# Performance work log

Hardware: AMD Instinct MI355X
Metric: run time of the kernel (lower is better)

Reference implementation:

```python
import jax, jax.numpy as jnp
import numpy as np

B, N = 4, 8192
D = 128
DEPTH = 4
LEAF = 32
HEADS = 4
HD = D // HEADS
SLOTS = 24
RANKS = [20, 32, 52, 82]                      # rank at encoder step j (fine -> coarse)
EXP = [RANKS[j] * (2 ** j) for j in range(DEPTH)]  # HODLR head output dims


def _rope_tables(seq_len, dim):
    inv_freq = 1.0 / (10000.0 ** (jnp.arange(0, dim, 2, dtype=jnp.float32) / dim))
    t = jnp.arange(seq_len, dtype=jnp.float32)
    freqs = t[:, None] * inv_freq[None, :]
    emb = jnp.concatenate([freqs, freqs], axis=-1)   # [S, dim]
    return jnp.cos(emb), jnp.sin(emb)


def _rotate_half(x):
    x1, x2 = jnp.split(x, 2, axis=-1)
    return jnp.concatenate([-x2, x1], axis=-1)


def _layernorm(x, g, b, eps=1e-5):
    mu = jnp.mean(x, -1, keepdims=True)
    var = jnp.mean((x - mu) ** 2, -1, keepdims=True)
    return (x - mu) * jax.lax.rsqrt(var + eps) * g + b


def _block_attn(h, qkv_w, qkv_b, pw, pb, cos, sin):
    Bc, Nc, C = h.shape
    nb = Nc // LEAF
    xb = h.reshape(Bc * nb, LEAF, C)
    qkv = (xb @ qkv_w + qkv_b).reshape(Bc * nb, LEAF, 3, HEADS, HD)
    qkv = qkv.transpose(2, 0, 3, 1, 4)               # [3, BN, H, L, hd]
    q, k, v = qkv[0], qkv[1], qkv[2]
    q = q * cos + _rotate_half(q) * sin              # full-dim RoPE (rope_dim == head_dim)
    k = k * cos + _rotate_half(k) * sin
    attn = jax.nn.softmax(jnp.einsum('bhqd,bhkd->bhqk', q, k) * (HD ** -0.5), axis=-1)
    o = jnp.einsum('bhqk,bhkd->bhqd', attn, v).transpose(0, 2, 1, 3).reshape(Bc * nb, LEAF, C)
    return (o @ pw + pb).reshape(Bc, Nc, C)


def _forward(x, cen_w, cen_b, nbr_w, nbr_b, inp_w, inp_b,
             leafp_w, leafp_b, leafh_w, leafh_b, log_scale_leaf,
             ln1_g, ln1_b, qkv_w, qkv_b, attnp_w, attnp_b,
             ln2_g, ln2_b, mlp1_w, mlp1_b, mlp2_w, mlp2_b, ds_w, ds_b,
             hu_w0, hu_b0, hv_w0, hv_b0, hu_w1, hu_b1, hv_w1, hv_b1,
             hu_w2, hu_b2, hv_w2, hv_b2, hu_w3, hu_b3, hv_w3, hv_b3):
    Bx, Nx, _ = x.shape
    # --- SymmetricNeighborEmbed (24 neighbor slots, vectorized) ---
    pos_i = x[..., 0:3]
    diag_i = x[..., 3:4]
    h_center = jnp.concatenate([pos_i, diag_i], -1) @ cen_w + cen_b          # [B,N,D]
    nb_feat = x[..., 4:4 + 5 * SLOTS].reshape(Bx, Nx, SLOTS, 5)
    rel = nb_feat[..., 0:1]
    pos_j = nb_feat[..., 1:4]
    w_ij = nb_feat[..., 4:5]
    active = (w_ij != 0.0).astype(x.dtype)
    feat = jnp.concatenate([rel * active, (pos_j - pos_i[:, :, None, :]) * active, w_ij], -1)
    e = (feat @ nbr_w + nbr_b) * active                                       # [B,N,24,D]
    h = h_center + jnp.sum(e, axis=2)
    h = h @ inp_w + inp_b
    # --- leaf dense diagonal blocks ---
    nl = Nx // LEAF
    hl = h.reshape(Bx, nl, LEAF, D) @ leafp_w + leafp_b                       # [B,nl,32,32]
    u_leaf = hl @ leafh_w + leafh_b
    dense = jnp.einsum('blik,bljk->blij', u_leaf, u_leaf) * jnp.exp(log_scale_leaf)
    diag_a = x[..., 3]                                                        # scale_A defaults to 1.0
    mask = jnp.abs(diag_a) > 1e-6
    new_diag = jnp.where(mask, 1.0 / jnp.where(mask, diag_a, 1.0), 1.0).reshape(Bx, nl, LEAF)
    dense = dense + new_diag[..., :, None] * jnp.eye(LEAF, dtype=x.dtype)
    # --- down-only encoder: transformer block -> HODLR head -> 2:1 downsample ---
    cos, sin = _rope_tables(LEAF, HD)
    hu = [(hu_w0, hu_b0), (hu_w1, hu_b1), (hu_w2, hu_b2), (hu_w3, hu_b3)]
    hv = [(hv_w0, hv_b0), (hv_w1, hv_b1), (hv_w2, hv_b2), (hv_w3, hv_b3)]
    us, vs = [], []
    for j in range(DEPTH):
        a = _block_attn(_layernorm(h, ln1_g[j], ln1_b[j]),
                        qkv_w[j], qkv_b[j], attnp_w[j], attnp_b[j], cos, sin)
        h = h + a
        m = _layernorm(h, ln2_g[j], ln2_b[j])
        m = jax.nn.gelu(m @ mlp1_w[j] + mlp1_b[j], approximate=False) @ mlp2_w[j] + mlp2_b[j]
        h = h + m
        us.append((h @ hu[j][0] + hu[j][1]).reshape(Bx, Nx, RANKS[j]))
        vs.append((h @ hv[j][0] + hv[j][1]).reshape(Bx, Nx, RANKS[j]))
        Bh, n, c = h.shape
        h = h.reshape(Bh, n // 2, 2 * c) @ ds_w[j] + ds_b[j]
    # single flat output: dense leaf blocks + all U/V HODLR factors
    return jnp.concatenate([dense.reshape(Bx, -1),
                            jnp.concatenate(us, -1).reshape(Bx, -1),
                            jnp.concatenate(vs, -1).reshape(Bx, -1)], -1)


def setup_inputs():
    key = jax.random.key(0)
    ks = iter(jax.random.split(key, 64))
    def rn(shape, s=0.05):
        return jax.random.normal(next(ks), shape, jnp.float32) * s
    z = lambda *s: jnp.zeros(s, jnp.float32)
    o = lambda *s: jnp.ones(s, jnp.float32)
    inp = {
        'x': jax.random.normal(next(ks), (B, N, 4 + 5 * SLOTS), jnp.float32),
        'cen_w': rn((4, D)), 'cen_b': z(D),
        'nbr_w': rn((5, D)), 'nbr_b': z(D),
        'inp_w': rn((D, D)), 'inp_b': z(D),
        'leafp_w': rn((D, LEAF)), 'leafp_b': z(LEAF),
        'leafh_w': rn((LEAF, LEAF), 0.01), 'leafh_b': z(LEAF),
        'log_scale_leaf': jnp.full((1,), np.log(0.01), jnp.float32),
        'ln1_g': o(DEPTH, D), 'ln1_b': z(DEPTH, D),
        'qkv_w': rn((DEPTH, D, 3 * D)), 'qkv_b': z(DEPTH, 3 * D),
        'attnp_w': rn((DEPTH, D, D)), 'attnp_b': z(DEPTH, D),
        'ln2_g': o(DEPTH, D), 'ln2_b': z(DEPTH, D),
        'mlp1_w': rn((DEPTH, D, 4 * D)), 'mlp1_b': z(DEPTH, 4 * D),
        'mlp2_w': rn((DEPTH, 4 * D, D)), 'mlp2_b': z(DEPTH, D),
        'ds_w': rn((DEPTH, 2 * D, D)), 'ds_b': z(DEPTH, D),
    }
    for j in range(DEPTH):
        inp['hu_w%d' % j] = rn((D, EXP[j]), 0.01)
        inp['hu_b%d' % j] = z(EXP[j])
        inp['hv_w%d' % j] = rn((D, EXP[j]), 0.01)
        inp['hv_b%d' % j] = z(EXP[j])
    return inp


def reference(x, cen_w, cen_b, nbr_w, nbr_b, inp_w, inp_b,
              leafp_w, leafp_b, leafh_w, leafh_b, log_scale_leaf,
              ln1_g, ln1_b, qkv_w, qkv_b, attnp_w, attnp_b,
              ln2_g, ln2_b, mlp1_w, mlp1_b, mlp2_w, mlp2_b, ds_w, ds_b,
              hu_w0, hu_b0, hv_w0, hv_b0, hu_w1, hu_b1, hv_w1, hv_b1,
              hu_w2, hu_b2, hv_w2, hv_b2, hu_w3, hu_b3, hv_w3, hv_b3):
    return _forward(x, cen_w, cen_b, nbr_w, nbr_b, inp_w, inp_b,
                    leafp_w, leafp_b, leafh_w, leafh_b, log_scale_leaf,
                    ln1_g, ln1_b, qkv_w, qkv_b, attnp_w, attnp_b,
                    ln2_g, ln2_b, mlp1_w, mlp1_b, mlp2_w, mlp2_b, ds_w, ds_b,
                    hu_w0, hu_b0, hv_w0, hv_b0, hu_w1, hu_b1, hv_w1, hv_b1,
                    hu_w2, hu_b2, hv_w2, hv_b2, hu_w3, hu_b3, hv_w3, hv_b3)
```

## Files before the change

kernel.cpp:

```cpp
#include <hip/hip_runtime.h>
#include <math.h>

#define DEV __device__ __forceinline__

constexpr int XFv = 124;
constexpr size_t OPB   = 3309568;
constexpr size_t UBASE = 262144;
constexpr size_t VBASE = 1785856;
constexpr int UVWID = 186;

using bfrag  = __attribute__((ext_vector_type(8))) short;
using f32x4v = __attribute__((ext_vector_type(4))) float;

DEV float* at4p(float* base, int t, int c0, int W) {
  return base + t * W + ((c0 + 4 * t) & (W - 1));
}
DEV float& at1r(float* base, int t, int c, int W) {
  return base[t * W + (((c & ~3) + 4 * t) & (W - 1)) + (c & 3)];
}
DEV float4 ld4g(const float* p) { return *(const float4*)p; }
DEV void fma4(float4& a, float s, const float4& w) {
  a.x += s * w.x; a.y += s * w.y; a.z += s * w.z; a.w += s * w.w;
}
DEV float gelu_fast(float x) {
// ... 66 lines not shown
  S[1280 + tid] = cb[tid];
  __syncthreads();
  float acc[11];
#pragma unroll
  for (int r = 0; r < 10; r++) acc[r] = 0.f;
  acc[10] = ib[tid];
  for (int k = 0; k < 128; k++) {
    float w = iw[k * 128 + tid];
#pragma unroll
    for (int r = 0; r < 11; r++) acc[r] += S[r * 128 + k] * w;
  }
#pragma unroll
  for (int r = 0; r < 11; r++) weff[r * 128 + tid] = acc[r];
  for (int idx = tid; idx < 512; idx += 128) {
    int pos = idx >> 4, d = idx & 15;
    float ang = (float)pos * expf(-0.57564627324851148f * (float)d);
    ropetab[idx] = cosf(ang);
    ropetab[512 + idx] = sinf(ang);
  }
}

__global__ __launch_bounds__(256) void node_embed2_kernel(
    const float* __restrict__ x, const float* __restrict__ weff,
    float* __restrict__ h) {
  __shared__ float XR[64 * XFv];
  __shared__ float RF[64][11];
  __shared__ __align__(16) float WE[11 * 128];
  int tid = threadIdx.x;
  int node0 = blockIdx.x * 64;
  for (int i = tid; i < 64 * XFv; i += 256)
    XR[i] = x[(size_t)node0 * XFv + i];
  for (int i = tid; i < 11 * 128; i += 256) WE[i] = weff[i];
  __syncthreads();
  {
    int nn = tid >> 2, sl = tid & 3;
    const float* xr = XR + nn * XFv;
    float p0 = xr[0], p1 = xr[1], p2 = xr[2];
    float g[6] = {0.f, 0.f, 0.f, 0.f, 0.f, 0.f};
#pragma unroll
    for (int s = 0; s < 6; s++) {
      const float* f = xr + 4 + 5 * (sl * 6 + s);
      float w = f[4];
      if (w != 0.0f) {
        g[0] += f[0]; g[1] += f[1] - p0; g[2] += f[2] - p1;
        g[3] += f[3] - p2; g[4] += w; g[5] += 1.0f;
      }
    }
#pragma unroll
    for (int i = 0; i < 6; i++) {
      g[i] += __shfl_xor(g[i], 1);
      g[i] += __shfl_xor(g[i], 2);
    }
    if (sl == 0) {
      RF[nn][0] = p0; RF[nn][1] = p1; RF[nn][2] = p2; RF[nn][3] = xr[3];
#pragma unroll
      for (int i = 0; i < 6; i++) RF[nn][4 + i] = g[i];
    }
  }
  __syncthreads();
  {
    int w = tid >> 6, lane = tid & 63;
    int c4 = lane & 31, hi = lane >> 5;
    const float4* WE4 = (const float4*)WE;
#pragma unroll
    for (int rr = 0; rr < 8; rr++) {
      int node = w * 16 + rr * 2 + hi;
      float4 acc = WE4[10 * 32 + c4];
#pragma unroll
      for (int f = 0; f < 10; f++)
        fma4(acc, RF[node][f], WE4[f * 32 + c4]);
      *(float4*)&h[(size_t)(node0 + node) * 128 + c4 * 4] = acc;
    }
  }
}

__global__ __launch_bounds__(256) void leaf_dense_kernel(
    const float* __restrict__ h, const float* __restrict__ x,
    const float* __restrict__ lpw, const float* __restrict__ lpb,
    const float* __restrict__ lhw, const float* __restrict__ lhb,
    const float* __restrict__ lsc, float* __restrict__ out) {
  __shared__ __align__(16) float HS[32 * 128];
  __shared__ __align__(16) float HL[32 * 32];
  __shared__ __align__(16) float UL[32 * 32];
  int tid = threadIdx.x;
  int leaf = blockIdx.x;
  size_t base = (size_t)leaf * (32 * 128);
  for (int i = tid; i < 32 * 128; i += 256) {
    int t = i >> 7, c = i & 127;
    at1r(HS, t, c, 128) = h[base + i];
  }
  __syncthreads();
  int t = tid & 31, cg = tid >> 5;
  {
    float4 acc = ld4g(&lpb[4 * cg]);
    for (int k4 = 0; k4 < 128; k4 += 4) {
      float4 xv = *(const float4*)at4p(HS, t, k4, 128);
      float xa[4] = {xv.x, xv.y, xv.z, xv.w};
#pragma unroll
      for (int kk = 0; kk < 4; kk++)
        fma4(acc, xa[kk], ld4g(&lpw[(k4 + kk) * 32 + 4 * cg]));
    }
    *(float4*)at4p(HL, t, 4 * cg, 32) = acc;
  }
  __syncthreads();
  {
    float4 acc = ld4g(&lhb[4 * cg]);
    for (int k4 = 0; k4 < 32; k4 += 4) {
      float4 xv = *(const float4*)at4p(HL, t, k4, 32);
      float xa[4] = {xv.x, xv.y, xv.z, xv.w};
#pragma unroll
      for (int kk = 0; kk < 4; kk++)
        fma4(acc, xa[kk], ld4g(&lhw[(k4 + kk) * 32 + 4 * cg]));
    }
    *(float4*)at4p(UL, t, 4 * cg, 32) = acc;
  }
  __syncthreads();
  {
    float scale = expf(lsc[0]);
    float acc[4] = {0.f, 0.f, 0.f, 0.f};
    for (int k4 = 0; k4 < 32; k4 += 4) {
      float4 xv = *(const float4*)at4p(UL, t, k4, 32);
      float xa[4] = {xv.x, xv.y, xv.z, xv.w};
#pragma unroll
      for (int kk = 0; kk < 4; kk++) {
        int k = k4 + kk;
#pragma unroll
        for (int i2 = 0; i2 < 4; i2++)
          acc[i2] += xa[kk] * at1r(UL, 4 * cg + i2, k, 32);
      }
    }
    int b = leaf >> 8, l = leaf & 255;
#pragma unroll
    for (int i2 = 0; i2 < 4; i2++) {
      int c = 4 * cg + i2;
      float v = acc[i2] * scale;
      if (c == t) {
        float dg = x[(size_t)(leaf * 32 + t) * XFv + 3];
        v += (fabsf(dg) > 1e-6f) ? (1.0f / dg) : 1.0f;
      }
      out[(size_t)b * OPB + (size_t)l * 1024 + t * 32 + c] = v;
    }
  }
}

__global__ __launch_bounds__(256, 4) void layer_mfma_kernel(
    float* __restrict__ h,
    const float* __restrict__ lng, const float* __restrict__ lnb,
    const ushort* __restrict__ wqkvt, const float* __restrict__ bqkv,
    const ushort* __restrict__ wpt, const float* __restrict__ pb,
    const float* __restrict__ rt,
    const float* __restrict__ ln2g, const float* __restrict__ ln2b,
    const ushort* __restrict__ w1t, const float* __restrict__ b1,
    const ushort* __restrict__ w2t, const float* __restrict__ b2) {
  __shared__ __align__(16) ushort SM[16384];
  ushort* XN = SM;
  ushort* QB = SM + 4096;
  ushort* KB = SM + 8192;
  ushort* VT = SM + 12288;
  float*  HS = (float*)(SM + 8192);
  int tid = threadIdx.x;
  size_t base = (size_t)blockIdx.x * (32 * 128);

  {
    int m = tid >> 3, p = tid & 7;
    const float* row = h + base + m * 128 + p * 16;
    float v[16];
    float s = 0.f;
#pragma unroll
    for (int i = 0; i < 16; i += 4) {
      float4 t4 = ld4g(row + i);
      v[i] = t4.x; v[i + 1] = t4.y; v[i + 2] = t4.z; v[i + 3] = t4.w;
      s += t4.x + t4.y + t4.z + t4.w;
    }
    s += __shfl_xor(s, 1); s += __shfl_xor(s, 2); s += __shfl_xor(s, 4);
    float mu = s * (1.0f / 128.0f);
    float s2 = 0.f;
#pragma unroll
    for (int i = 0; i < 16; i++) { float d = v[i] - mu; s2 += d * d; }
    s2 += __shfl_xor(s2, 1); s2 += __shfl_xor(s2, 2); s2 += __shfl_xor(s2, 4);
    float rs = rsqrtf(s2 * (1.0f / 128.0f) + 1e-5f);
    unsigned* XW = (unsigned*)XN;
#pragma unroll
    for (int i = 0; i < 16; i += 2) {
      int c = p * 16 + i;
      float x0 = (v[i] - mu) * rs * lng[c] + lnb[c];
      float x1 = (v[i + 1] - mu) * rs * lng[c + 1] + lnb[c + 1];
      int kp = c >> 1;
      XW[m * 64 + ((kp + 4 * m) & 63)] =
          (unsigned)f2bf(x0) | ((unsigned)f2bf(x1) << 16);
    }
  }
  __syncthreads();

  int w = tid >> 6, l = tid & 63, lm = l & 15, q = l >> 4;

  {
    f32x4v acc[2][6];
#pragma unroll
    for (int mt = 0; mt < 2; mt++)
#pragma unroll
      for (int nt = 0; nt < 6; nt++) acc[mt][nt] = (f32x4v){0.f, 0.f, 0.f, 0.f};
    for (int ks = 0; ks < 4; ks++) {
      bfrag a[2];
#pragma unroll
      for (int mt = 0; mt < 2; mt++) {
        int mm = mt * 16 + lm;
        a[mt] = *(const bfrag*)&XN[mm * 128 + ((ks * 32 + q * 8 + 8 * mm) & 127)];
      }
#pragma unroll
      for (int nt = 0; nt < 6; nt++) {
        int n = w * 96 + nt * 16 + lm;
        bfrag b = *(const bfrag*)&wqkvt[(size_t)n * 128 + ks * 32 + q * 8];
#pragma unroll
        for (int mt = 0; mt < 2; mt++)
          acc[mt][nt] = __builtin_amdgcn_mfma_f32_16x16x32_bf16(
              a[mt], b, acc[mt][nt], 0, 0, 0);
      }
    }
    float csA[4] = {}, snA[4] = {}, csB[4] = {}, snB[4] = {};
    if (w < 3) {
#pragma unroll
      for (int r = 0; r < 4; r++) {
        int pa = q * 4 + r;
        csA[r] = rt[pa * 16 + lm];        snA[r] = rt[512 + pa * 16 + lm];
        csB[r] = rt[(pa + 16) * 16 + lm]; snB[r] = rt[512 + (pa + 16) * 16 + lm];
      }
    }
#pragma unroll
    for (int p2 = 0; p2 < 3; p2++) {
      int g = w * 6 + 2 * p2;
      int ne = g * 16 + lm;
      if (g < 16) {
        float be = bqkv[ne], bo = bqkv[ne + 16];
        ushort* dst = (g < 8) ? QB : KB;
        int de = (g < 8) ? ne : ne - 128;
#pragma unroll
        for (int mt = 0; mt < 2; mt++)
#pragma unroll
          for (int r = 0; r < 4; r++) {
            int mm = mt * 16 + q * 4 + r;
            float cs = (mt & 1) ? csB[r] : csA[r];
            float sn = (mt & 1) ? snB[r] : snA[r];
            float e = acc[mt][2 * p2][r] + be;
            float o = acc[mt][2 * p2 + 1][r] + bo;
            stb128(dst, mm, de, e * cs - o * sn);
            stb128(dst, mm, de + 16, o * cs + e * sn);
          }
      } else {
#pragma unroll
        for (int h2 = 0; h2 < 2; h2++) {
          int nt = 2 * p2 + h2;
          int nv = (g + h2) * 16 + lm;
          int dv = nv - 256;
          float bv = bqkv[nv];
#pragma unroll
          for (int mt = 0; mt < 2; mt++) {
            int t0 = mt * 16 + q * 4;
            short4 pk;
            pk.x = (short)f2bf(acc[mt][nt][0] + bv);
            pk.y = (short)f2bf(acc[mt][nt][1] + bv);
            pk.z = (short)f2bf(acc[mt][nt][2] + bv);
            pk.w = (short)f2bf(acc[mt][nt][3] + bv);
            *(short4*)&VT[dv * 32 + (((t0 & ~7) + 8 * dv) & 31) + (t0 & 7)] = pk;
          }
        }
      }
    }
  }
  __syncthreads();

  ushort* SP = XN;
  {
    int head = w;
    f32x4v sc[2][2];
#pragma unroll
    for (int a2 = 0; a2 < 2; a2++)
#pragma unroll
      for (int b2 = 0; b2 < 2; b2++) sc[a2][b2] = (f32x4v){0.f, 0.f, 0.f, 0.f};
    bfrag qa[2], kb[2];
#pragma unroll
    for (int mt2 = 0; mt2 < 2; mt2++) {
      int row = mt2 * 16 + lm;
      qa[mt2] = *(const bfrag*)&QB[row * 128 + ((head * 32 + q * 8 + 8 * row) & 127)];
    }
#pragma unroll
    for (int nt2 = 0; nt2 < 2; nt2++) {
      int kt = nt2 * 16 + lm;
      kb[nt2] = *(const bfrag*)&KB[kt * 128 + ((head * 32 + q * 8 + 8 * kt) & 127)];
    }
#pragma unroll
    for (int mt2 = 0; mt2 < 2; mt2++)
#pragma unroll
      for (int nt2 = 0; nt2 < 2; nt2++)
        sc[mt2][nt2] = __builtin_amdgcn_mfma_f32_16x16x32_bf16(
            qa[mt2], kb[nt2], sc[mt2][nt2], 0, 0, 0);
    const float scl = 0.17677669529663688f;
#pragma unroll
    for (int mt2 = 0; mt2 < 2; mt2++)
#pragma unroll
      for (int nt2 = 0; nt2 < 2; nt2++)
#pragma unroll
        for (int r = 0; r < 4; r++) {
          int qt = mt2 * 16 + q * 4 + r;
          int kc = nt2 * 16 + lm;
          SP[head * 1024 + qt * 32 + (((kc & ~7) + 8 * qt) & 31) + (kc & 7)] =
              f2bf(sc[mt2][nt2][r] * scl);
        }
  }
  __syncthreads();

  {
    if (tid < 128) {
      int head = tid >> 5, qt = tid & 31;
      ushort* rowp = SP + head * 1024 + qt * 32;
      float v[32];
#pragma unroll
      for (int pc = 0; pc < 4; pc++) {
        uint4 ch = *(const uint4*)&rowp[pc * 8];
        unsigned uu[4] = {ch.x, ch.y, ch.z, ch.w};
#pragma unroll
        for (int i2 = 0; i2 < 4; i2++) {
          v[pc * 8 + 2 * i2]     = __uint_as_float(uu[i2] << 16);
          v[pc * 8 + 2 * i2 + 1] = __uint_as_float(uu[i2] & 0xffff0000u);
        }
      }
      float mx = -1e30f;
#pragma unroll
      for (int i = 0; i < 32; i++) mx = fmaxf(mx, v[i]);
      float s = 0.f;
#pragma unroll
      for (int i = 0; i < 32; i++) { v[i] = __expf(v[i] - mx); s += v[i]; }
      float inv = 1.0f / s;
#pragma unroll
      for (int pc = 0; pc < 4; pc++) {
        uint4 ch;
        unsigned uu[4];
#pragma unroll
        for (int i2 = 0; i2 < 4; i2++)
          uu[i2] = (unsigned)f2bf(v[pc * 8 + 2 * i2] * inv) |
                   ((unsigned)f2bf(v[pc * 8 + 2 * i2 + 1] * inv) << 16);
        ch.x = uu[0]; ch.y = uu[1]; ch.z = uu[2]; ch.w = uu[3];
        *(uint4*)&rowp[pc * 8] = ch;
      }
    }
  }
  __syncthreads();

  ushort* OB = QB;
  {
    int head = w;
    f32x4v ov[2][2];
#pragma unroll
    for (int a2 = 0; a2 < 2; a2++)
#pragma unroll
      for (int b2 = 0; b2 < 2; b2++) ov[a2][b2] = (f32x4v){0.f, 0.f, 0.f, 0.f};
    bfrag pa[2], vb2[2];
#pragma unroll
    for (int mt2 = 0; mt2 < 2; mt2++) {
      int qt = mt2 * 16 + lm;
      pa[mt2] = *(const bfrag*)&SP[head * 1024 + qt * 32 + ((q * 8 + 8 * qt) & 31)];
    }
#pragma unroll
    for (int nt2 = 0; nt2 < 2; nt2++) {
      int gdim = head * 32 + nt2 * 16 + lm;
      vb2[nt2] = *(const bfrag*)&VT[gdim * 32 + ((q * 8 + 8 * gdim) & 31)];
    }
#pragma unroll
    for (int mt2 = 0; mt2 < 2; mt2++)
#pragma unroll
      for (int nt2 = 0; nt2 < 2; nt2++)
        ov[mt2][nt2] = __builtin_amdgcn_mfma_f32_16x16x32_bf16(
            pa[mt2], vb2[nt2], ov[mt2][nt2], 0, 0, 0);
#pragma unroll
    for (int mt2 = 0; mt2 < 2; mt2++)
#pragma unroll
      for (int nt2 = 0; nt2 < 2; nt2++)
#pragma unroll
        for (int r = 0; r < 4; r++) {
          int qt = mt2 * 16 + q * 4 + r;
          int gdim = head * 32 + nt2 * 16 + lm;
          stb128(OB, qt, gdim, ov[mt2][nt2][r]);
        }
  }
  __syncthreads();

  {
    f32x4v po[2][2];
#pragma unroll
    for (int mt = 0; mt < 2; mt++)
#pragma unroll
      for (int nt = 0; nt < 2; nt++) po[mt][nt] = (f32x4v){0.f, 0.f, 0.f, 0.f};
    for (int ks = 0; ks < 4; ks++) {
      bfrag a[2];
#pragma unroll
      for (int mt = 0; mt < 2; mt++) {
        int mm = mt * 16 + lm;
        a[mt] = *(const bfrag*)&OB[mm * 128 + ((ks * 32 + q * 8 + 8 * mm) & 127)];
      }
#pragma unroll
      for (int nt = 0; nt < 2; nt++) {
        int n = w * 32 + nt * 16 + lm;
        bfrag b = *(const bfrag*)&wpt[(size_t)n * 128 + ks * 32 + q * 8];
#pragma unroll
        for (int mt = 0; mt < 2; mt++)
          po[mt][nt] = __builtin_amdgcn_mfma_f32_16x16x32_bf16(
              a[mt], b, po[mt][nt], 0, 0, 0);
      }
    }
#pragma unroll
    for (int nt = 0; nt < 2; nt++) {
      int n = w * 32 + nt * 16 + lm;
      float bv = pb[n];
#pragma unroll
      for (int mt = 0; mt < 2; mt++)
#pragma unroll
        for (int r = 0; r < 4; r++) {
          int mm = mt * 16 + q * 4 + r;
          at1r(HS, mm, n, 128) = po[mt][nt][r] + bv;
        }
    }
  }
  __syncthreads();

  {
    int j = tid & 31;
    int c0 = j * 4;
    float g0 = ln2g[c0], g1 = ln2g[c0 + 1], g2 = ln2g[c0 + 2], g3 = ln2g[c0 + 3];
    float e0 = ln2b[c0], e1 = ln2b[c0 + 1], e2 = ln2b[c0 + 2], e3 = ln2b[c0 + 3];
    unsigned* XW = (unsigned*)XN;
#pragma unroll
    for (int k2 = 0; k2 < 4; k2++) {
      int idx = tid + 256 * k2;
      int tok = idx >> 5;
      float4 hg = ld4g(&h[base + (size_t)idx * 4]);
      float4 ao = *(const float4*)at4p(HS, tok, 4 * j, 128);
      float4 hn;
      hn.x = hg.x + ao.x; hn.y = hg.y + ao.y;
      hn.z = hg.z + ao.z; hn.w = hg.w + ao.w;
      *(float4*)at4p(HS, tok, 4 * j, 128) = hn;
      float s = hn.x + hn.y + hn.z + hn.w;
      s += __shfl_xor(s, 1); s += __shfl_xor(s, 2); s += __shfl_xor(s, 4);
      s += __shfl_xor(s, 8); s += __shfl_xor(s, 16);
      float mu = s * (1.0f / 128.0f);
      float d0 = hn.x - mu, d1 = hn.y - mu, d2 = hn.z - mu, d3 = hn.w - mu;
      float s2 = d0 * d0 + d1 * d1 + d2 * d2 + d3 * d3;
      s2 += __shfl_xor(s2, 1); s2 += __shfl_xor(s2, 2); s2 += __shfl_xor(s2, 4);
      s2 += __shfl_xor(s2, 8); s2 += __shfl_xor(s2, 16);
      float rs = rsqrtf(s2 * (1.0f / 128.0f) + 1e-5f);
      float x0 = d0 * rs * g0 + e0;
      float x1 = d1 * rs * g1 + e1;
      float x2 = d2 * rs * g2 + e2;
      float x3 = d3 * rs * g3 + e3;
      int kp = 2 * j;
      XW[tok * 64 + ((kp + 4 * tok) & 63)] =
          (unsigned)f2bf(x0) | ((unsigned)f2bf(x1) << 16);
      XW[tok * 64 + ((kp + 1 + 4 * tok) & 63)] =
          (unsigned)f2bf(x2) | ((unsigned)f2bf(x3) << 16);
    }
  }
  __syncthreads();

  ushort* HC = QB;
  f32x4v acc2[2][2];
#pragma unroll
  for (int mt = 0; mt < 2; mt++)
#pragma unroll
    for (int nt = 0; nt < 2; nt++) acc2[mt][nt] = (f32x4v){0.f, 0.f, 0.f, 0.f};

  for (int hc = 0; hc < 4; hc++) {
    f32x4v acc1[2][2];
#pragma unroll
    for (int mt = 0; mt < 2; mt++)
#pragma unroll
      for (int nt = 0; nt < 2; nt++) acc1[mt][nt] = (f32x4v){0.f, 0.f, 0.f, 0.f};
#pragma unroll
    for (int ks = 0; ks < 4; ks++) {
      bfrag a[2];
#pragma unroll
      for (int mt = 0; mt < 2; mt++) {
        int mm = mt * 16 + lm;
        a[mt] = *(const bfrag*)&XN[mm * 128 + ((ks * 32 + q * 8 + 8 * mm) & 127)];
      }
#pragma unroll
      for (int nt = 0; nt < 2; nt++) {
        int n = hc * 128 + w * 32 + nt * 16 + lm;
        bfrag b = *(const bfrag*)&w1t[(size_t)n * 128 + ks * 32 + q * 8];
#pragma unroll
        for (int mt = 0; mt < 2; mt++)
          acc1[mt][nt] = __builtin_amdgcn_mfma_f32_16x16x32_bf16(
              a[mt], b, acc1[mt][nt], 0, 0, 0);
      }
    }
    if (hc) __syncthreads();
#pragma unroll
    for (int nt = 0; nt < 2; nt++) {
      int nl = w * 32 + nt * 16 + lm;
      float b1v = b1[hc * 128 + nl];
#pragma unroll
      for (int mt = 0; mt < 2; mt++)
#pragma unroll
        for (int r = 0; r < 4; r++) {
          int mm = mt * 16 + q * 4 + r;
          float val = gelu_fast(acc1[mt][nt][r] + b1v);
          HC[mm * 128 + (((nl & ~7) + 8 * mm) & 127) + (nl & 7)] = f2bf(val);
        }
    }
    __syncthreads();
#pragma unroll
    for (int ks = 0; ks < 4; ks++) {
      bfrag a[2];
#pragma unroll
      for (int mt = 0; mt < 2; mt++) {
        int mm = mt * 16 + lm;
        a[mt] = *(const bfrag*)&HC[mm * 128 + ((ks * 32 + q * 8 + 8 * mm) & 127)];
      }
#pragma unroll
      for (int nt = 0; nt < 2; nt++) {
        int n = w * 32 + nt * 16 + lm;
        bfrag b = *(const bfrag*)&w2t[(size_t)n * 512 + hc * 128 + ks * 32 + q * 8];
#pragma unroll
        for (int mt = 0; mt < 2; mt++)
          acc2[mt][nt] = __builtin_amdgcn_mfma_f32_16x16x32_bf16(
              a[mt], b, acc2[mt][nt], 0, 0, 0);
      }
    }
  }

#pragma unroll
  for (int nt = 0; nt < 2; nt++) {
    int n = w * 32 + nt * 16 + lm;
    float b2v = b2[n];
#pragma unroll
    for (int mt = 0; mt < 2; mt++)
#pragma unroll
      for (int r = 0; r < 4; r++) {
        int mm = mt * 16 + q * 4 + r;
        h[base + (size_t)mm * 128 + n] = at1r(HS, mm, n, 128) + acc2[mt][nt][r] + b2v;
      }
  }
}

template <int EXPJ, int RANK, int LVL, int NSPLIT>
__global__ __launch_bounds__(256) void uvds_kernel(
    const float* __restrict__ h,
    const ushort* __restrict__ uwt, const float* __restrict__ ub,
    const ushort* __restrict__ vwt, const float* __restrict__ vb,
    float* __restrict__ ustg, float* __restrict__ vstg,
    float* __restrict__ hout,
    const ushort* __restrict__ dwt, const float* __restrict__ dsb) {
  constexpr int NT16 = (EXPJ + 15) / 16;
  constexpr int NJOBS = 2 * NT16;
  __shared__ __align__(16) ushort XN[64 * 128];
  int tid = threadIdx.x;
  int t0 = blockIdx.x * 64;
  size_t base = (size_t)t0 * 128;
  {
    int m = tid >> 2, p = tid & 3;
    const float* row = h + base + m * 128 + p * 32;
    unsigned* XW = (unsigned*)XN;
#pragma unroll
    for (int i = 0; i < 32; i += 4) {
      float4 t4 = ld4g(row + i);
      int kp = (p * 32 + i) >> 1;
      XW[m * 64 + ((kp + 4 * m) & 63)] =
          (unsigned)f2bf(t4.x) | ((unsigned)f2bf(t4.y) << 16);
      XW[m * 64 + ((kp + 1 + 4 * m) & 63)] =
          (unsigned)f2bf(t4.z) | ((unsigned)f2bf(t4.w) << 16);
    }
  }
  __syncthreads();
  int w = tid >> 6, l = tid & 63, lm = l & 15, q = l >> 4;
  int gw = w + 4 * blockIdx.y;
  for (int jj = gw; jj < NJOBS; jj += 4 * NSPLIT) {
    int uvsel = jj & 1, nt = jj >> 1;
    const ushort* wt = uvsel ? vwt : uwt;
    const float* bias = uvsel ? vb : ub;
    float* stg = uvsel ? vstg : ustg;
    f32x4v acc[4];
#pragma unroll
    for (int mt = 0; mt < 4; mt++) acc[mt] = (f32x4v){0.f, 0.f, 0.f, 0.f};
    for (int ks = 0; ks < 4; ks++) {
      bfrag b = *(const bfrag*)&wt[(size_t)(nt * 16 + lm) * 128 + ks * 32 + q * 8];
#pragma unroll
      for (int mt = 0; mt < 4; mt++) {
        int mm = mt * 16 + lm;
        int ke = ks * 32 + q * 8;
        bfrag a = *(const bfrag*)&XN[mm * 128 + ((ke + 8 * mm) & 127)];
        acc[mt] = __builtin_amdgcn_mfma_f32_16x16x32_bf16(a, b, acc[mt], 0, 0, 0);
      }
    }
    int c = nt * 16 + lm;
    if (c < EXPJ) {
      float bv = bias[c];
#pragma unroll
      for (int mt = 0; mt < 4; mt++)
#pragma unroll
        for (int r = 0; r < 4; r++) {
          int mm = mt * 16 + q * 4 + r;
          stg[(size_t)(t0 + mm) * EXPJ + c] = acc[mt][r] + bv;
        }
    }
  }
  if constexpr (LVL < 3) {
    if (blockIdx.y == 0) {
      f32x4v dacc[2][2];
#pragma unroll
      for (int mt = 0; mt < 2; mt++)
#pragma unroll
        for (int nt = 0; nt < 2; nt++) dacc[mt][nt] = (f32x4v){0.f, 0.f, 0.f, 0.f};
      for (int ks = 0; ks < 8; ks++) {
        bfrag a[2];
#pragma unroll
        for (int mt = 0; mt < 2; mt++) {
          int rr = mt * 16 + lm;
          int tok = 2 * rr + (ks >> 2);
          int c2 = (ks & 3) * 32 + q * 8;
          a[mt] = *(const bfrag*)&XN[tok * 128 + ((c2 + 8 * tok) & 127)];
        }
#pragma unroll
        for (int nt = 0; nt < 2; nt++) {
          int n = w * 32 + nt * 16 + lm;
          bfrag b = *(const bfrag*)&dwt[(size_t)n * 256 + ks * 32 + q * 8];
#pragma unroll
          for (int mt = 0; mt < 2; mt++)
            dacc[mt][nt] = __builtin_amdgcn_mfma_f32_16x16x32_bf16(
                a[mt], b, dacc[mt][nt], 0, 0, 0);
        }
      }
      size_t ob2 = (size_t)blockIdx.x * (32 * 128);
#pragma unroll
      for (int nt = 0; nt < 2; nt++) {
        int n = w * 32 + nt * 16 + lm;
        float bv = dsb[n];
#pragma unroll
        for (int mt = 0; mt < 2; mt++)
#pragma unroll
          for (int r = 0; r < 4; r++) {
            int mm = mt * 16 + q * 4 + r;
            hout[ob2 + (size_t)mm * 128 + n] = dacc[mt][nt][r] + bv;
          }
      }
    }
  }
}

struct StgPtrs { const float* u[4]; const float* v[4]; };
__global__ __launch_bounds__(256) void uv_assemble_kernel(
    StgPtrs sp, float* __restrict__ out) {
  __shared__ unsigned char JL[93];
  __shared__ unsigned char CM[93];
  int tid = threadIdx.x;
  if (tid < 93) {
    int c = 2 * tid;
    int j = (c < 20) ? 0 : (c < 52) ? 1 : (c < 104) ? 2 : 3;
    int coff = (j == 0) ? 0 : (j == 1) ? 20 : (j == 2) ? 52 : 104;
    JL[tid] = (unsigned char)j;
    CM[tid] = (unsigned char)(c - coff);
  }
  __syncthreads();
  int g0 = blockIdx.x * 32;
  for (int i = tid; i < 32 * 93; i += 256) {
    int rr = i / 93, cp = i - rr * 93;
    int g = g0 + rr;
    int b = g >> 13, n = g & 8191;
    int j = JL[cp], cm = CM[cp];
    int expj, rank;
    if (j == 0)      { expj = 20;  rank = 20; }
    else if (j == 1) { expj = 64;  rank = 32; }
    else if (j == 2) { expj = 208; rank = 52; }
    else             { expj = 656; rank = 82; }
    int tok = (b << (13 - j)) + (n >> j);
    int cdiv = n & ((1 << j) - 1);
    size_t si = (size_t)tok * expj + cdiv * rank + cm;
    size_t ob = (size_t)b * OPB + (size_t)n * UVWID + 2 * cp;
    *(float2*)&out[ob + UBASE] = *(const float2*)&sp.u[j][si];
    *(float2*)&out[ob + VBASE] = *(const float2*)&sp.v[j][si];
  }
}

// ... 127 lines not shown
```

Baseline: 441.0 us.

## Double-buffer MLP hidden chunks and prefetch weight fragments in fused layer kernel

Restructures the transformer layer kernel's MLP into a software pipeline. A second LDS buffer holds GELU chunks, so the next chunk's first matmul overlaps the previous chunk's second matmul and the loop needs one fewer barrier per chunk. It also prefetches proj and first MLP1 weight fragments into registers before the attention stages, keeps the input residual in registers instead of reloading it from global for LN2, and splits softmax rows across two threads so all 256 threads work. LDS rises from 32KB to 40KB and register pressure grows, which may reduce occupancy under launch_bounds(256,4).

```diff
diff --git a/kernel.cpp b/kernel.cpp
--- a/kernel.cpp
+++ b/kernel.cpp
@@ -242,47 +242,47 @@
     const float* __restrict__ ln2g, const float* __restrict__ ln2b,
     const ushort* __restrict__ w1t, const float* __restrict__ b1,
     const ushort* __restrict__ w2t, const float* __restrict__ b2) {
-  __shared__ __align__(16) ushort SM[16384];
+  __shared__ __align__(16) ushort SM[20480];
   ushort* XN = SM;
   ushort* QB = SM + 4096;
   ushort* KB = SM + 8192;
   ushort* VT = SM + 12288;
+  ushort* HC1 = SM + 16384;
   float*  HS = (float*)(SM + 8192);
   int tid = threadIdx.x;
   size_t base = (size_t)blockIdx.x * (32 * 128);
-
-  {
-    int m = tid >> 3, p = tid & 7;
-    const float* row = h + base + m * 128 + p * 16;
-    float v[16];
+  int m8 = tid >> 3, p8 = tid & 7;
+  int w = tid >> 6, l = tid & 63, lm = l & 15, q = l >> 4;
+  float hreg[16];
+
+  {
+    const float* row = h + base + m8 * 128 + p8 * 16;
     float s = 0.f;
 #pragma unroll
     for (int i = 0; i < 16; i += 4) {
       float4 t4 = ld4g(row + i);
-      v[i] = t4.x; v[i + 1] = t4.y; v[i + 2] = t4.z; v[i + 3] = t4.w;
+      hreg[i] = t4.x; hreg[i + 1] = t4.y; hreg[i + 2] = t4.z; hreg[i + 3] = t4.w;
       s += t4.x + t4.y + t4.z + t4.w;
     }
     s += __shfl_xor(s, 1); s += __shfl_xor(s, 2); s += __shfl_xor(s, 4);
     float mu = s * (1.0f / 128.0f);
     float s2 = 0.f;
 #pragma unroll
-    for (int i = 0; i < 16; i++) { float d = v[i] - mu; s2 += d * d; }
+    for (int i = 0; i < 16; i++) { float d = hreg[i] - mu; s2 += d * d; }
     s2 += __shfl_xor(s2, 1); s2 += __shfl_xor(s2, 2); s2 += __shfl_xor(s2, 4);
     float rs = rsqrtf(s2 * (1.0f / 128.0f) + 1e-5f);
     unsigned* XW = (unsigned*)XN;
 #pragma unroll
     for (int i = 0; i < 16; i += 2) {
-      int c = p * 16 + i;
-      float x0 = (v[i] - mu) * rs * lng[c] + lnb[c];
-      float x1 = (v[i + 1] - mu) * rs * lng[c + 1] + lnb[c + 1];
+      int c = p8 * 16 + i;
+      float x0 = (hreg[i] - mu) * rs * lng[c] + lnb[c];
+      float x1 = (hreg[i + 1] - mu) * rs * lng[c + 1] + lnb[c + 1];
       int kp = c >> 1;
-      XW[m * 64 + ((kp + 4 * m) & 63)] =
+      XW[m8 * 64 + ((kp + 4 * m8) & 63)] =
           (unsigned)f2bf(x0) | ((unsigned)f2bf(x1) << 16);
     }
   }
   __syncthreads();
-
-  int w = tid >> 6, l = tid & 63, lm = l & 15, q = l >> 4;
 
   {
     f32x4v acc[2][6];
@@ -359,6 +359,15 @@
   }
   __syncthreads();
 
+  bfrag pfF[4][2];
+#pragma unroll
+  for (int ks = 0; ks < 4; ks++)
+#pragma unroll
+    for (int nt = 0; nt < 2; nt++) {
+      int n = w * 32 + nt * 16 + lm;
+      pfF[ks][nt] = *(const bfrag*)&wpt[(size_t)n * 128 + ks * 32 + q * 8];
+    }
+
   ushort* SP = XN;
   {
     int head = w;
@@ -400,38 +409,39 @@
   __syncthreads();
 
   {
-    if (tid < 128) {
-      int head = tid >> 5, qt = tid & 31;
-      ushort* rowp = SP + head * 1024 + qt * 32;
-      float v[32];
-#pragma unroll
-      for (int pc = 0; pc < 4; pc++) {
-        uint4 ch = *(const uint4*)&rowp[pc * 8];
-        unsigned uu[4] = {ch.x, ch.y, ch.z, ch.w};
-#pragma unroll
-        for (int i2 = 0; i2 < 4; i2++) {
-          v[pc * 8 + 2 * i2]     = __uint_as_float(uu[i2] << 16);
-          v[pc * 8 + 2 * i2 + 1] = __uint_as_float(uu[i2] & 0xffff0000u);
-        }
-      }
-      float mx = -1e30f;
-#pragma unroll
-      for (int i = 0; i < 32; i++) mx = fmaxf(mx, v[i]);
-      float s = 0.f;
-#pragma unroll
-      for (int i = 0; i < 32; i++) { v[i] = __expf(v[i] - mx); s += v[i]; }
-      float inv = 1.0f / s;
-#pragma unroll
-      for (int pc = 0; pc < 4; pc++) {
-        uint4 ch;
-        unsigned uu[4];
-#pragma unroll
-        for (int i2 = 0; i2 < 4; i2++)
-          uu[i2] = (unsigned)f2bf(v[pc * 8 + 2 * i2] * inv) |
-                   ((unsigned)f2bf(v[pc * 8 + 2 * i2 + 1] * inv) << 16);
-        ch.x = uu[0]; ch.y = uu[1]; ch.z = uu[2]; ch.w = uu[3];
-        *(uint4*)&rowp[pc * 8] = ch;
-      }
+    int rowid = tid >> 1, half = tid & 1;
+    int head = rowid >> 5, qt = rowid & 31;
+    ushort* rowp = SP + head * 1024 + qt * 32 + half * 16;
+    float v[16];
+#pragma unroll
+    for (int pc = 0; pc < 2; pc++) {
+      uint4 ch = *(const uint4*)&rowp[pc * 8];
+      unsigned uu[4] = {ch.x, ch.y, ch.z, ch.w};
+#pragma unroll
+      for (int i2 = 0; i2 < 4; i2++) {
+        v[pc * 8 + 2 * i2]     = __uint_as_float(uu[i2] << 16);
+        v[pc * 8 + 2 * i2 + 1] = __uint_as_float(uu[i2] & 0xffff0000u);
+      }
+    }
+    float mx = -1e30f;
+#pragma unroll
+    for (int i = 0; i < 16; i++) mx = fmaxf(mx, v[i]);
+    mx = fmaxf(mx, __shfl_xor(mx, 1));
+    float s = 0.f;
+#pragma unroll
+    for (int i = 0; i < 16; i++) { v[i] = __expf(v[i] - mx); s += v[i]; }
+    s += __shfl_xor(s, 1);
+    float inv = 1.0f / s;
+#pragma unroll
+    for (int pc = 0; pc < 2; pc++) {
+      uint4 ch;
+      unsigned uu[4];
+#pragma unroll
+      for (int i2 = 0; i2 < 4; i2++)
+        uu[i2] = (unsigned)f2bf(v[pc * 8 + 2 * i2] * inv) |
+                 ((unsigned)f2bf(v[pc * 8 + 2 * i2 + 1] * inv) << 16);
+      ch.x = uu[0]; ch.y = uu[1]; ch.z = uu[2]; ch.w = uu[3];
+      *(uint4*)&rowp[pc * 8] = ch;
     }
   }
   __syncthreads();
@@ -480,6 +490,7 @@
     for (int mt = 0; mt < 2; mt++)
 #pragma unroll
       for (int nt = 0; nt < 2; nt++) po[mt][nt] = (f32x4v){0.f, 0.f, 0.f, 0.f};
+#pragma unroll
     for (int ks = 0; ks < 4; ks++) {
       bfrag a[2];
 #pragma unroll
@@ -488,14 +499,11 @@
         a[mt] = *(const bfrag*)&OB[mm * 128 + ((ks * 32 + q * 8 + 8 * mm) & 127)];
       }
 #pragma unroll
-      for (int nt = 0; nt < 2; nt++) {
-        int n = w * 32 + nt * 16 + lm;
-        bfrag b = *(const bfrag*)&wpt[(size_t)n * 128 + ks * 32 + q * 8];
+      for (int nt = 0; nt < 2; nt++)
 #pragma unroll
         for (int mt = 0; mt < 2; mt++)
           po[mt][nt] = __builtin_amdgcn_mfma_f32_16x16x32_bf16(
-              a[mt], b, po[mt][nt], 0, 0, 0);
-      }
+              a[mt], pfF[ks][nt], po[mt][nt], 0, 0, 0);
     }
 #pragma unroll
     for (int nt = 0; nt < 2; nt++) {
@@ -512,57 +520,63 @@
   }
   __syncthreads();
 
-  {
-    int j = tid & 31;
-    int c0 = j * 4;
-    float g0 = ln2g[c0], g1 = ln2g[c0 + 1], g2 = ln2g[c0 + 2], g3 = ln2g[c0 + 3];
-    float e0 = ln2b[c0], e1 = ln2b[c0 + 1], e2 = ln2b[c0 + 2], e3 = ln2b[c0 + 3];
+  bfrag pfW1[4][2];
+#pragma unroll
+  for (int ks = 0; ks < 4; ks++)
+#pragma unroll
+    for (int nt = 0; nt < 2; nt++) {
+      int n = w * 32 + nt * 16 + lm;
+      pfW1[ks][nt] = *(const bfrag*)&w1t[(size_t)n * 128 + ks * 32 + q * 8];
+    }
+
+  {
+    float s = 0.f;
+    float hn[16];
+#pragma unroll
+    for (int i = 0; i < 16; i += 4) {
+      float4 ao = *(const float4*)at4p(HS, m8, p8 * 16 + i, 128);
+      hn[i] = hreg[i] + ao.x;     hn[i + 1] = hreg[i + 1] + ao.y;
+      hn[i + 2] = hreg[i + 2] + ao.z; hn[i + 3] = hreg[i + 3] + ao.w;
+      s += hn[i] + hn[i + 1] + hn[i + 2] + hn[i + 3];
+    }
+    s += __shfl_xor(s, 1); s += __shfl_xor(s, 2); s += __shfl_xor(s, 4);
+    float mu = s * (1.0f / 128.0f);
+    float s2 = 0.f;
+#pragma unroll
+    for (int i = 0; i < 16; i++) { float d = hn[i] - mu; s2 += d * d; }
+    s2 += __shfl_xor(s2, 1); s2 += __shfl_xor(s2, 2); s2 += __shfl_xor(s2, 4);
+    float rs = rsqrtf(s2 * (1.0f / 128.0f) + 1e-5f);
+#pragma unroll
+    for (int i = 0; i < 16; i += 4) {
+      float4 w4;
+      w4.x = hn[i]; w4.y = hn[i + 1]; w4.z = hn[i + 2]; w4.w = hn[i + 3];
+      *(float4*)at4p(HS, m8, p8 * 16 + i, 128) = w4;
+    }
     unsigned* XW = (unsigned*)XN;
 #pragma unroll
-    for (int k2 = 0; k2 < 4; k2++) {
-      int idx = tid + 256 * k2;
-      int tok = idx >> 5;
-      float4 hg = ld4g(&h[base + (size_t)idx * 4]);
-      float4 ao = *(const float4*)at4p(HS, tok, 4 * j, 128);
-      float4 hn;
-      hn.x = hg.x + ao.x; hn.y = hg.y + ao.y;
-      hn.z = hg.z + ao.z; hn.w = hg.w + ao.w;
-      *(float4*)at4p(HS, tok, 4 * j, 128) = hn;
-      float s = hn.x + hn.y + hn.z + hn.w;
-      s += __shfl_xor(s, 1); s += __shfl_xor(s, 2); s += __shfl_xor(s, 4);
-      s += __shfl_xor(s, 8); s += __shfl_xor(s, 16);
-      float mu = s * (1.0f / 128.0f);
-      float d0 = hn.x - mu, d1 = hn.y - mu, d2 = hn.z - mu, d3 = hn.w - mu;
-      float s2 = d0 * d0 + d1 * d1 + d2 * d2 + d3 * d3;
-      s2 += __shfl_xor(s2, 1); s2 += __shfl_xor(s2, 2); s2 += __shfl_xor(s2, 4);
-      s2 += __shfl_xor(s2, 8); s2 += __shfl_xor(s2, 16);
-      float rs = rsqrtf(s2 * (1.0f / 128.0f) + 1e-5f);
-      float x0 = d0 * rs * g0 + e0;
-      float x1 = d1 * rs * g1 + e1;
-      float x2 = d2 * rs * g2 + e2;
-      float x3 = d3 * rs * g3 + e3;
-      int kp = 2 * j;
-      XW[tok * 64 + ((kp + 4 * tok) & 63)] =
+    for (int i = 0; i < 16; i += 2) {
+      int c = p8 * 16 + i;
+      float x0 = (hn[i] - mu) * rs * ln2g[c] + ln2b[c];
+      float x1 = (hn[i + 1] - mu) * rs * ln2g[c + 1] + ln2b[c + 1];
+      int kp = c >> 1;
+      XW[m8 * 64 + ((kp + 4 * m8) & 63)] =
           (unsigned)f2bf(x0) | ((unsigned)f2bf(x1) << 16);
-      XW[tok * 64 + ((kp + 1 + 4 * tok) & 63)] =
-          (unsigned)f2bf(x2) | ((unsigned)f2bf(x3) << 16);
-    }
-  }
-  __syncthreads();
-
-  ushort* HC = QB;
+    }
+  }
+  __syncthreads();
+
+  ushort* HC0 = QB;
   f32x4v acc2[2][2];
 #pragma unroll
   for (int mt = 0; mt < 2; mt++)
 #pragma unroll
     for (int nt = 0; nt < 2; nt++) acc2[mt][nt] = (f32x4v){0.f, 0.f, 0.f, 0.f};
 
-  for (int hc = 0; hc < 4; hc++) {
-    f32x4v acc1[2][2];
+  auto mlp1_calc = [&](int hc, f32x4v A1[2][2]) {
 #pragma unroll
     for (int mt = 0; mt < 2; mt++)
 #pragma unroll
-      for (int nt = 0; nt < 2; nt++) acc1[mt][nt] = (f32x4v){0.f, 0.f, 0.f, 0.f};
+      for (int nt = 0; nt < 2; nt++) A1[mt][nt] = (f32x4v){0.f, 0.f, 0.f, 0.f};
 #pragma unroll
     for (int ks = 0; ks < 4; ks++) {
       bfrag a[2];
@@ -577,11 +591,12 @@
         bfrag b = *(const bfrag*)&w1t[(size_t)n * 128 + ks * 32 + q * 8];
 #pragma unroll
         for (int mt = 0; mt < 2; mt++)
-          acc1[mt][nt] = __builtin_amdgcn_mfma_f32_16x16x32_bf16(
-              a[mt], b, acc1[mt][nt], 0, 0, 0);
-      }
-    }
-    if (hc) __syncthreads();
+          A1[mt][nt] = __builtin_amdgcn_mfma_f32_16x16x32_bf16(
+              a[mt], b, A1[mt][nt], 0, 0, 0);
+      }
+    }
+  };
+  auto gelu_store = [&](int hc, f32x4v A1[2][2], ushort* HCd) {
 #pragma unroll
     for (int nt = 0; nt < 2; nt++) {
       int nl = w * 32 + nt * 16 + lm;
@@ -591,18 +606,19 @@
 #pragma unroll
         for (int r = 0; r < 4; r++) {
           int mm = mt * 16 + q * 4 + r;
-          float val = gelu_fast(acc1[mt][nt][r] + b1v);
-          HC[mm * 128 + (((nl & ~7) + 8 * mm) & 127) + (nl & 7)] = f2bf(val);
+          float val = gelu_fast(A1[mt][nt][r] + b1v);
+          HCd[mm * 128 + (((nl & ~7) + 8 * mm) & 127) + (nl & 7)] = f2bf(val);
         }
     }
-    __syncthreads();
+  };
+  auto mlp2_calc = [&](int hc, ushort* HCr) {
 #pragma unroll
     for (int ks = 0; ks < 4; ks++) {
       bfrag a[2];
 #pragma unroll
       for (int mt = 0; mt < 2; mt++) {
         int mm = mt * 16 + lm;
-        a[mt] = *(const bfrag*)&HC[mm * 128 + ((ks * 32 + q * 8 + 8 * mm) & 127)];
+        a[mt] = *(const bfrag*)&HCr[mm * 128 + ((ks * 32 + q * 8 + 8 * mm) & 127)];
       }
 #pragma unroll
       for (int nt = 0; nt < 2; nt++) {
@@ -614,7 +630,45 @@
               a[mt], b, acc2[mt][nt], 0, 0, 0);
       }
     }
-  }
+  };
+
+  f32x4v a1A[2][2], a1B[2][2];
+  {
+#pragma unroll
+    for (int mt = 0; mt < 2; mt++)
+#pragma unroll
+      for (int nt = 0; nt < 2; nt++) a1A[mt][nt] = (f32x4v){0.f, 0.f, 0.f, 0.f};
+#pragma unroll
+    for (int ks = 0; ks < 4; ks++) {
+      bfrag a[2];
+#pragma unroll
+      for (int mt = 0; mt < 2; mt++) {
+        int mm = mt * 16 + lm;
+        a[mt] = *(const bfrag*)&XN[mm * 128 + ((ks * 32 + q * 8 + 8 * mm) & 127)];
+      }
+#pragma unroll
+      for (int nt = 0; nt < 2; nt++)
+#pragma unroll
+        for (int mt = 0; mt < 2; mt++)
+          a1A[mt][nt] = __builtin_amdgcn_mfma_f32_16x16x32_bf16(
+              a[mt], pfW1[ks][nt], a1A[mt][nt], 0, 0, 0);
+    }
+  }
+  gelu_store(0, a1A, HC0);
+  __syncthreads();
+  mlp1_calc(1, a1B);
+  mlp2_calc(0, HC0);
+  gelu_store(1, a1B, HC1);
+  __syncthreads();
+  mlp1_calc(2, a1A);
+  mlp2_calc(1, HC1);
+  gelu_store(2, a1A, HC0);
+  __syncthreads();
+  mlp1_calc(3, a1B);
+  mlp2_calc(2, HC0);
+  gelu_store(3, a1B, HC1);
+  __syncthreads();
+  mlp2_calc(3, HC1);
 
 #pragma unroll
   for (int nt = 0; nt < 2; nt++) {
```

After: 434.9 us. No clear change (-1.4%).

## Double-buffer MLP hidden chunks and split softmax rows across thread pairs

Applied to the files above, without the earlier changes.

The MLP loop now ping-pongs between two LDS buffers for the GELU hidden chunk. This lets the next chunk's first GEMM be issued alongside the current chunk's second GEMM, and drops from two barriers per chunk to one. Softmax now uses all 256 threads, with two threads per row combining max and sum through shuffles, instead of 128 idle-half threads. LDS per block grows from 32 KB to 40 KB, which may reduce occupancy under the 4-blocks launch bound.

```diff
diff --git a/kernel.cpp b/kernel.cpp
--- a/kernel.cpp
+++ b/kernel.cpp
@@ -242,18 +242,20 @@
     const float* __restrict__ ln2g, const float* __restrict__ ln2b,
     const ushort* __restrict__ w1t, const float* __restrict__ b1,
     const ushort* __restrict__ w2t, const float* __restrict__ b2) {
-  __shared__ __align__(16) ushort SM[16384];
+  __shared__ __align__(16) ushort SM[20480];
   ushort* XN = SM;
   ushort* QB = SM + 4096;
   ushort* KB = SM + 8192;
   ushort* VT = SM + 12288;
+  ushort* HC1 = SM + 16384;
   float*  HS = (float*)(SM + 8192);
   int tid = threadIdx.x;
   size_t base = (size_t)blockIdx.x * (32 * 128);
-
-  {
-    int m = tid >> 3, p = tid & 7;
-    const float* row = h + base + m * 128 + p * 16;
+  int w = tid >> 6, l = tid & 63, lm = l & 15, q = l >> 4;
+
+  {
+    int m8 = tid >> 3, p8 = tid & 7;
+    const float* row = h + base + m8 * 128 + p8 * 16;
     float v[16];
     float s = 0.f;
 #pragma unroll
@@ -272,17 +274,15 @@
     unsigned* XW = (unsigned*)XN;
 #pragma unroll
     for (int i = 0; i < 16; i += 2) {
-      int c = p * 16 + i;
+      int c = p8 * 16 + i;
       float x0 = (v[i] - mu) * rs * lng[c] + lnb[c];
       float x1 = (v[i + 1] - mu) * rs * lng[c + 1] + lnb[c + 1];
       int kp = c >> 1;
-      XW[m * 64 + ((kp + 4 * m) & 63)] =
+      XW[m8 * 64 + ((kp + 4 * m8) & 63)] =
           (unsigned)f2bf(x0) | ((unsigned)f2bf(x1) << 16);
     }
   }
   __syncthreads();
-
-  int w = tid >> 6, l = tid & 63, lm = l & 15, q = l >> 4;
 
   {
     f32x4v acc[2][6];
@@ -400,38 +400,39 @@
   __syncthreads();
 
   {
-    if (tid < 128) {
-      int head = tid >> 5, qt = tid & 31;
-      ushort* rowp = SP + head * 1024 + qt * 32;
-      float v[32];
-#pragma unroll
-      for (int pc = 0; pc < 4; pc++) {
-        uint4 ch = *(const uint4*)&rowp[pc * 8];
-        unsigned uu[4] = {ch.x, ch.y, ch.z, ch.w};
-#pragma unroll
-        for (int i2 = 0; i2 < 4; i2++) {
-          v[pc * 8 + 2 * i2]     = __uint_as_float(uu[i2] << 16);
-          v[pc * 8 + 2 * i2 + 1] = __uint_as_float(uu[i2] & 0xffff0000u);
-        }
-      }
-      float mx = -1e30f;
-#pragma unroll
-      for (int i = 0; i < 32; i++) mx = fmaxf(mx, v[i]);
-      float s = 0.f;
-#pragma unroll
-      for (int i = 0; i < 32; i++) { v[i] = __expf(v[i] - mx); s += v[i]; }
-      float inv = 1.0f / s;
-#pragma unroll
-      for (int pc = 0; pc < 4; pc++) {
-        uint4 ch;
-        unsigned uu[4];
-#pragma unroll
-        for (int i2 = 0; i2 < 4; i2++)
-          uu[i2] = (unsigned)f2bf(v[pc * 8 + 2 * i2] * inv) |
-                   ((unsigned)f2bf(v[pc * 8 + 2 * i2 + 1] * inv) << 16);
-        ch.x = uu[0]; ch.y = uu[1]; ch.z = uu[2]; ch.w = uu[3];
-        *(uint4*)&rowp[pc * 8] = ch;
-      }
+    int rowid = tid >> 1, half = tid & 1;
+    int head = rowid >> 5, qt = rowid & 31;
+    ushort* rowp = SP + head * 1024 + qt * 32 + half * 16;
+    float v[16];
+#pragma unroll
+    for (int pc = 0; pc < 2; pc++) {
+      uint4 ch = *(const uint4*)&rowp[pc * 8];
+      unsigned uu[4] = {ch.x, ch.y, ch.z, ch.w};
+#pragma unroll
+      for (int i2 = 0; i2 < 4; i2++) {
+        v[pc * 8 + 2 * i2]     = __uint_as_float(uu[i2] << 16);
+        v[pc * 8 + 2 * i2 + 1] = __uint_as_float(uu[i2] & 0xffff0000u);
+      }
+    }
+    float mx = -1e30f;
+#pragma unroll
+    for (int i = 0; i < 16; i++) mx = fmaxf(mx, v[i]);
+    mx = fmaxf(mx, __shfl_xor(mx, 1));
+    float s = 0.f;
+#pragma unroll
+    for (int i = 0; i < 16; i++) { v[i] = __expf(v[i] - mx); s += v[i]; }
+    s += __shfl_xor(s, 1);
+    float inv = 1.0f / s;
+#pragma unroll
+    for (int pc = 0; pc < 2; pc++) {
+      uint4 ch;
+      unsigned uu[4];
+#pragma unroll
+      for (int i2 = 0; i2 < 4; i2++)
+        uu[i2] = (unsigned)f2bf(v[pc * 8 + 2 * i2] * inv) |
+                 ((unsigned)f2bf(v[pc * 8 + 2 * i2 + 1] * inv) << 16);
+      ch.x = uu[0]; ch.y = uu[1]; ch.z = uu[2]; ch.w = uu[3];
+      *(uint4*)&rowp[pc * 8] = ch;
     }
   }
   __syncthreads();
@@ -550,19 +551,18 @@
   }
   __syncthreads();
 
-  ushort* HC = QB;
+  ushort* HC0 = QB;
   f32x4v acc2[2][2];
 #pragma unroll
   for (int mt = 0; mt < 2; mt++)
 #pragma unroll
     for (int nt = 0; nt < 2; nt++) acc2[mt][nt] = (f32x4v){0.f, 0.f, 0.f, 0.f};
 
-  for (int hc = 0; hc < 4; hc++) {
-    f32x4v acc1[2][2];
+  auto mlp1_calc = [&](int hc, f32x4v A1[2][2]) {
 #pragma unroll
     for (int mt = 0; mt < 2; mt++)
 #pragma unroll
-      for (int nt = 0; nt < 2; nt++) acc1[mt][nt] = (f32x4v){0.f, 0.f, 0.f, 0.f};
+      for (int nt = 0; nt < 2; nt++) A1[mt][nt] = (f32x4v){0.f, 0.f, 0.f, 0.f};
 #pragma unroll
     for (int ks = 0; ks < 4; ks++) {
       bfrag a[2];
@@ -577,11 +577,12 @@
         bfrag b = *(const bfrag*)&w1t[(size_t)n * 128 + ks * 32 + q * 8];
 #pragma unroll
         for (int mt = 0; mt < 2; mt++)
-          acc1[mt][nt] = __builtin_amdgcn_mfma_f32_16x16x32_bf16(
-              a[mt], b, acc1[mt][nt], 0, 0, 0);
-      }
-    }
-    if (hc) __syncthreads();
+          A1[mt][nt] = __builtin_amdgcn_mfma_f32_16x16x32_bf16(
+              a[mt], b, A1[mt][nt], 0, 0, 0);
+      }
+    }
+  };
+  auto gelu_store = [&](int hc, f32x4v A1[2][2], ushort* HCd) {
 #pragma unroll
     for (int nt = 0; nt < 2; nt++) {
       int nl = w * 32 + nt * 16 + lm;
@@ -591,18 +592,19 @@
 #pragma unroll
         for (int r = 0; r < 4; r++) {
           int mm = mt * 16 + q * 4 + r;
-          float val = gelu_fast(acc1[mt][nt][r] + b1v);
-          HC[mm * 128 + (((nl & ~7) + 8 * mm) & 127) + (nl & 7)] = f2bf(val);
+          float val = gelu_fast(A1[mt][nt][r] + b1v);
+          HCd[mm * 128 + (((nl & ~7) + 8 * mm) & 127) + (nl & 7)] = f2bf(val);
         }
     }
-    __syncthreads();
+  };
+  auto mlp2_calc = [&](int hc, ushort* HCr) {
 #pragma unroll
     for (int ks = 0; ks < 4; ks++) {
       bfrag a[2];
 #pragma unroll
       for (int mt = 0; mt < 2; mt++) {
         int mm = mt * 16 + lm;
-        a[mt] = *(const bfrag*)&HC[mm * 128 + ((ks * 32 + q * 8 + 8 * mm) & 127)];
+        a[mt] = *(const bfrag*)&HCr[mm * 128 + ((ks * 32 + q * 8 + 8 * mm) & 127)];
       }
 #pragma unroll
       for (int nt = 0; nt < 2; nt++) {
@@ -614,7 +616,25 @@
               a[mt], b, acc2[mt][nt], 0, 0, 0);
       }
     }
-  }
+  };
+
+  f32x4v a1A[2][2], a1B[2][2];
+  mlp1_calc(0, a1A);
+  gelu_store(0, a1A, HC0);
+  __syncthreads();
+  mlp1_calc(1, a1B);
+  mlp2_calc(0, HC0);
+  gelu_store(1, a1B, HC1);
+  __syncthreads();
+  mlp1_calc(2, a1A);
+  mlp2_calc(1, HC1);
+  gelu_store(2, a1A, HC0);
+  __syncthreads();
+  mlp1_calc(3, a1B);
+  mlp2_calc(2, HC0);
+  gelu_store(3, a1B, HC1);
+  __syncthreads();
+  mlp2_calc(3, HC1);
 
 #pragma unroll
   for (int nt = 0; nt < 2; nt++) {
```

New measurement: 419.7 us. 4.8% less time.
